# Performance work log

Hardware: AMD Instinct MI355X
Metric: run time of the kernel (lower is better)

Reference implementation:

```python
import jax, jax.numpy as jnp
import numpy as np
import math

D_MODEL = 1024
D_STATE = 64
DT_MIN = 0.001
DT_MAX = 0.1
BATCH = 4
SEQLEN = 4096


def make_hippo_matrix(N):
    P = np.sqrt(1 + 2 * np.arange(N))
    A = P[:, np.newaxis] * P[np.newaxis, :]
    A = np.tril(A) - np.diag(np.arange(N))
    return jnp.asarray(-A, dtype=jnp.float32)


def setup_inputs() -> dict:
    key = jax.random.key(0)
    k_u, k_B, k_C, k_D, k_dt = jax.random.split(key, 5)
    u = jax.random.normal(k_u, (BATCH, SEQLEN, D_MODEL), dtype=jnp.float32)
    A = make_hippo_matrix(D_STATE)  # (N, N) HiPPO-LegS buffer
    B = jax.random.normal(k_B, (D_STATE, 1), dtype=jnp.float32)
    C = jax.random.normal(k_C, (1, D_STATE), dtype=jnp.float32)
    D = jax.random.normal(k_D, (1,), dtype=jnp.float32)
    log_dt = (jax.random.uniform(k_dt, (1,), dtype=jnp.float32)
              * (math.log(DT_MAX) - math.log(DT_MIN)) + math.log(DT_MIN))
    return {"u": u, "A": A, "B": B, "C": C, "D": D, "log_dt": log_dt}


def _forward(u, A, B, C, D, log_dt):
    n = A.shape[0]
    dt = jnp.exp(log_dt)[0]
    A_bar = jax.scipy.linalg.expm(dt * A)                     # (N, N)
    B_bar = jnp.linalg.solve(A, (A_bar - jnp.eye(n, dtype=A.dtype)) @ B)  # (N, 1)
    bvec = B_bar[:, 0]          # (N,)
    cvec = C[0]                 # (N,)
    d_scalar = D[0]
    # Faithful to source: only channel 0 of u drives the SSM.
    u0 = u[:, :, 0]             # (Bn, L)

    def step(x, u_t):
        # x: (Bn, N), u_t: (Bn,)
        x = x @ A_bar.T + u_t[:, None] * bvec
        y = x @ cvec + d_scalar * u_t   # (Bn,)
        return x, y

    x0 = jnp.zeros((u.shape[0], n), dtype=u.dtype)
    _, ys = jax.lax.scan(step, x0, jnp.swapaxes(u0, 0, 1))   # (L, Bn)
    # Scalar output broadcast across all H channels (matches torch expand)
    y = jnp.broadcast_to(jnp.swapaxes(ys, 0, 1)[:, :, None], u.shape)
    return y


def reference(u, A, B, C, D, log_dt):
    return _forward(u, A, B, C, D, log_dt)
```

## Files before the change

### kernel.cpp

```cpp
#include <hip/hip_runtime.h>


#define NT 1024
#define MP 68
#define MB (64 * MP)

typedef __attribute__((ext_vector_type(8))) short v8s;
typedef __attribute__((ext_vector_type(4))) float v4f;

__device__ __forceinline__ unsigned short bf16r(float x) {
  union { float f; unsigned u; } v; v.f = x;
  unsigned r = v.u + 0x7fffu + ((v.u >> 16) & 1u);
  return (unsigned short)(r >> 16);
}
__device__ __forceinline__ float bf2f(unsigned short h) {
  union { unsigned u; float f; } v; v.u = ((unsigned)h) << 16;
  return v.f;
}

__device__ void mm(const float* Ag, const float* Bs, int bT,
                   float* Cd, int cpitch, float* Cd2,
                   int nrt, int nct, int rowbase, int colbase,
                   unsigned short* FRAG) {
  const int t = threadIdx.x;
  __syncthreads();
  {
    const int slot = t >> 1;
    const int jh = (t & 1) * 4;
    const int l = slot & 63;
    const int Tq = slot >> 6;
    const int mrow = (Tq >> 1) * 16 + (l & 15);
    const int kk = (Tq & 1) * 32 + (l >> 4) * 8 + jh;
    const float4 f = *(const float4*)(Ag + mrow * MP + kk);
    ushort4 H, L;
    unsigned short h;
    h = bf16r(f.x); H.x = h; L.x = bf16r(f.x - bf2f(h));
    h = bf16r(f.y); H.y = h; L.y = bf16r(f.y - bf2f(h));
    h = bf16r(f.z); H.z = h; L.z = bf16r(f.z - bf2f(h));
    h = bf16r(f.w); H.w = h; L.w = bf16r(f.w - bf2f(h));
    *(ushort4*)(FRAG + slot * 8 + jh) = H;
    *(ushort4*)(FRAG + 4096 + slot * 8 + jh) = L;
    float y0, y1, y2, y3;
    if (bT) {
      const float4 g = *(const float4*)(Bs + mrow * MP + kk);
      y0 = g.x; y1 = g.y; y2 = g.z; y3 = g.w;
    } else {
      y0 = Bs[(kk + 0) * MP + mrow]; y1 = Bs[(kk + 1) * MP + mrow];
      y2 = Bs[(kk + 2) * MP + mrow]; y3 = Bs[(kk + 3) * MP + mrow];
    }
    h = bf16r(y0); H.x = h; L.x = bf16r(y0 - bf2f(h));
    h = bf16r(y1); H.y = h; L.y = bf16r(y1 - bf2f(h));
    h = bf16r(y2); H.z = h; L.z = bf16r(y2 - bf2f(h));
    h = bf16r(y3); H.w = h; L.w = bf16r(y3 - bf2f(h));
    *(ushort4*)(FRAG + 8192 + slot * 8 + jh) = H;
    *(ushort4*)(FRAG + 12288 + slot * 8 + jh) = L;
  }
  __syncthreads();
  {
    const int w = t >> 6, l = t & 63;
    if (w < 4 && w < nrt) {
      const v8s Ah0 = *(const v8s*)(FRAG + ((w * 2 + 0) * 64 + l) * 8);
      const v8s Ah1 = *(const v8s*)(FRAG + ((w * 2 + 1) * 64 + l) * 8);
      const v8s Al0 = *(const v8s*)(FRAG + 4096 + ((w * 2 + 0) * 64 + l) * 8);
      const v8s Al1 = *(const v8s*)(FRAG + 4096 + ((w * 2 + 1) * 64 + l) * 8);
      for (int Cc = 0; Cc < nct; ++Cc) {
        const v8s Bh0 = *(const v8s*)(FRAG + 8192 + ((Cc * 2 + 0) * 64 + l) * 8);
        const v8s Bh1 = *(const v8s*)(FRAG + 8192 + ((Cc * 2 + 1) * 64 + l) * 8);
        const v8s Bl0 = *(const v8s*)(FRAG + 12288 + ((Cc * 2 + 0) * 64 + l) * 8);
        const v8s Bl1 = *(const v8s*)(FRAG + 12288 + ((Cc * 2 + 1) * 64 + l) * 8);
        v4f acc = {0.f, 0.f, 0.f, 0.f};
        acc = __builtin_amdgcn_mfma_f32_16x16x32_bf16(Ah0, Bh0, acc, 0, 0, 0);
        acc = __builtin_amdgcn_mfma_f32_16x16x32_bf16(Ah1, Bh1, acc, 0, 0, 0);
        acc = __builtin_amdgcn_mfma_f32_16x16x32_bf16(Ah0, Bl0, acc, 0, 0, 0);
        acc = __builtin_amdgcn_mfma_f32_16x16x32_bf16(Ah1, Bl1, acc, 0, 0, 0);
        acc = __builtin_amdgcn_mfma_f32_16x16x32_bf16(Al0, Bh0, acc, 0, 0, 0);
        acc = __builtin_amdgcn_mfma_f32_16x16x32_bf16(Al1, Bh1, acc, 0, 0, 0);
        const int col = colbase + Cc * 16 + (l & 15);
        const int r0 = rowbase + w * 16 + (l >> 4) * 4;
        Cd[(r0 + 0) * cpitch + col] = acc[0];
        Cd[(r0 + 1) * cpitch + col] = acc[1];
        Cd[(r0 + 2) * cpitch + col] = acc[2];
        Cd[(r0 + 3) * cpitch + col] = acc[3];
        if (Cd2) {
          Cd2[(r0 + 0) * MP + col] = acc[0];
          Cd2[(r0 + 1) * MP + col] = acc[1];
          Cd2[(r0 + 2) * MP + col] = acc[2];
          Cd2[(r0 + 3) * MP + col] = acc[3];
        }
      }
    }
  }
  __syncthreads();
}

__device__ __forceinline__ void mv64row(const float* M, const float* vin,
                                        float* vout, float* vscr) {
  __syncthreads();
  const int t = threadIdx.x, i = t & 63, c = t >> 6;
  const float4 m = *(const float4*)(M + i * MP + c * 4);
  vscr[t] = fmaf(m.x, vin[c * 4 + 0], fmaf(m.y, vin[c * 4 + 1],
            fmaf(m.z, vin[c * 4 + 2], m.w * vin[c * 4 + 3])));
  __syncthreads();
  if (t < 64) {
    float s = 0.f;
#pragma unroll
    for (int cc = 0; cc < 16; ++cc) s += vscr[cc * 64 + t];
    vout[t] = s;
  }
  __syncthreads();
}

__device__ __forceinline__ void mv64colT(const float* M, const float* vin,
                                         float* vout, float* vscr) {
  __syncthreads();
  const int t = threadIdx.x, i = t & 63, c = t >> 6;
  float p = 0.f;
#pragma unroll
  for (int j = 0; j < 4; ++j) p = fmaf(M[(c * 4 + j) * MP + i], vin[c * 4 + j], p);
  vscr[t] = p;
  __syncthreads();
  if (t < 64) {
    float s = 0.f;
#pragma unroll
    for (int cc = 0; cc < 16; ++cc) s += vscr[cc * 64 + t];
    vout[t] = s;
  }
  __syncthreads();
}

__device__ void buildG(float* dst, const float* X, const float* X2, const float* X3,
                       float c0, float c1, float c2, float c3, const float* addsrc) {
  __syncthreads();
  for (int e = threadIdx.x; e < MB; e += NT) {
    const int r = e / MP, c = e - r * MP;
    if (c < 64) {
      float v = c1 * X[e] + c2 * X2[e] + c3 * X3[e];
      if (r == c) v += c0;
      if (addsrc) v += addsrc[e];
      dst[e] = v;
    }
  }
  __syncthreads();
}

__global__ __launch_bounds__(NT) void s4_setup(const float* __restrict__ u,
    const float* __restrict__ A, const float* __restrict__ Bv,
    const float* __restrict__ Cv, const float* __restrict__ logdt,
    float* __restrict__ ws) {
  if (blockIdx.x > 0) {
    const int idx = (blockIdx.x - 1) * NT + threadIdx.x;
    ws[4096 + idx] = u[(size_t)idx * 1024];
    return;
  }
  __shared__ __align__(16) float S0[MB];
  __shared__ __align__(16) unsigned short FRAG[16384];
  __shared__ float vB[64], v1[64], v2[64], v3[64], va[64], vb[64], vg[64];
  __shared__ int s_s;
  float* vscr = (float*)FRAG;

  const int t = threadIdx.x;
  float* kbuf = ws;
  float* gX   = ws + 20480;
  float* gX2  = ws + 24832;
  float* gX3  = ws + 29184;
  float* gU0  = ws + 33536;
  float* gU1  = ws + 37888;
  float* gBRT = ws + 42240;
  float* gCQT = ws + 46592;
  const float dt = expf(logdt[0]);

  const float invf[17] = {1.f, 1.f, 1.f / 2.f, 1.f / 6.f, 1.f / 24.f, 1.f / 120.f,
                          1.f / 720.f, 1.f / 5040.f, 1.f / 40320.f, 1.f / 362880.f,
                          1.f / 3628800.f, 1.f / 39916800.f, 1.f / 479001600.f,
                          1.f / 6.2270208e9f, 1.f / 8.71782912e10f,
                          1.f / 1.307674368e12f, 1.f / 2.0922789888e13f};

  {
    const int j = t & 63, ch = t >> 6;
    float p = 0.f;
#pragma unroll
    for (int ii = 0; ii < 4; ++ii) p += fabsf(A[(ch * 4 + ii) * 64 + j]);
    vscr[t] = p;
    __syncthreads();
    if (t < 64) {
      float cs = 0.f;
#pragma unroll
      for (int c = 0; c < 16; ++c) cs += vscr[c * 64 + t];
      cs *= dt;
#pragma unroll
      for (int off = 32; off > 0; off >>= 1) cs = fmaxf(cs, __shfl_xor(cs, off));
      if (t == 0) {
        int s = 0;
        while (cs > 2.0f && s < 30) { cs *= 0.5f; ++s; }
        s_s = s;
      }
    }
    __syncthreads();
  }
  const int sq = s_s;
  const float scl = ldexpf(dt, -sq);

  {
    const float4 a4 = *(const float4*)(A + t * 4);
    float4 x;
    x.x = a4.x * scl; x.y = a4.y * scl; x.z = a4.z * scl; x.w = a4.w * scl;
    const int r = t >> 4, c4 = (t & 15) * 4;
    *(float4*)(S0 + r * MP + c4) = x;
    *(float4*)(gX + r * MP + c4) = x;
  }
  if (t < 64) vB[t] = Bv[t];

  mm(S0, S0, 0, S0, MP, gX2, 4, 4, 0, 0, FRAG);
  mm(gX, S0, 0, gX3, MP, nullptr, 4, 4, 0, 0, FRAG);
  mm(S0, S0, 0, S0, MP, nullptr, 4, 4, 0, 0, FRAG);

  mv64row(gX,  vB, v1, vscr);
  mv64row(gX2, vB, v2, vscr);
  mv64row(gX3, vB, v3, vscr);
  if (t < 64)
    va[t] = invf[13] * vB[t] + invf[14] * v1[t] + invf[15] * v2[t] + invf[16] * v3[t];
  mv64row(S0, va, vb, vscr);
  if (t < 64)
    va[t] = invf[9] * vB[t] + invf[10] * v1[t] + invf[11] * v2[t] + invf[12] * v3[t] + vb[t];
  mv64row(S0, va, vb, vscr);
  if (t < 64)
    va[t] = invf[5] * vB[t] + invf[6] * v1[t] + invf[7] * v2[t] + invf[8] * v3[t] + vb[t];
  mv64row(S0, va, vb, vscr);
  if (t < 64)
    vg[t] = invf[1] * vB[t] + invf[2] * v1[t] + invf[3] * v2[t] + invf[4] * v3[t] + vb[t];

  buildG(gU0, gX, gX2, gX3, invf[12], invf[13], invf[14], invf[15], nullptr);
  mm(gU0, S0, 0, gU1, MP, nullptr, 4, 4, 0, 0, FRAG);
  buildG(gU1, gX, gX2, gX3, invf[8], invf[9], invf[10], invf[11], gU1);
  mm(gU1, S0, 0, gU0, MP, nullptr, 4, 4, 0, 0, FRAG);
  buildG(gU0, gX, gX2, gX3, invf[4], invf[5], invf[6], invf[7], gU0);
  mm(gU0, S0, 0, S0, MP, nullptr, 4, 4, 0, 0, FRAG);
  buildG(S0, gX, gX2, gX3, invf[0], invf[1], invf[2], invf[3], S0);

  for (int it = 0; it < sq; ++it) {
    mv64row(S0, vg, va, vscr);
    if (t < 64) vg[t] = 0.5f * (va[t] + vg[t]);
    mm(S0, S0, 0, S0, MP, nullptr, 4, 4, 0, 0, FRAG);
  }

  __syncthreads();
  if (t < 64) { va[t] = dt * vg[t]; gBRT[t] = dt * vg[t]; }
  {
    float* vc = va; float* vn = vb;
    for (int r = 1; r < 16; ++r) {
      mv64row(S0, vc, vn, vscr);
      if (t < 64) gBRT[r * MP + t] = vn[t];
      float* tmp = vc; vc = vn; vn = tmp;
    }
  }

  mm(S0, S0, 0, S0, MP, nullptr, 4, 4, 0, 0, FRAG);
  mm(S0, S0, 0, S0, MP, nullptr, 4, 4, 0, 0, FRAG);
  mm(S0, S0, 0, S0, MP, nullptr, 4, 4, 0, 0, FRAG);
  mm(S0, S0, 0, S0, MP, nullptr, 4, 4, 0, 0, FRAG);
  mm(gBRT, S0, 1, gBRT, MP, nullptr, 1, 4, 16, 0, FRAG);
  mm(S0, S0, 0, S0, MP, nullptr, 4, 4, 0, 0, FRAG);
  mm(gBRT, S0, 1, gBRT, MP, nullptr, 2, 4, 32, 0, FRAG);
  mm(S0, S0, 0, S0, MP, nullptr, 4, 4, 0, 0, FRAG);

  __syncthreads();
  if (t < 64) { va[t] = Cv[t]; gCQT[t] = Cv[t]; }
  {
    float* vc = va; float* vn = vb;
    for (int qx = 1; qx < 16; ++qx) {
      mv64colT(S0, vc, vn, vscr);
      if (t < 64) gCQT[qx * MP + t] = vn[t];
      float* tmp = vc; vc = vn; vn = tmp;
    }
  }

  mm(S0, S0, 0, S0, MP, nullptr, 4, 4, 0, 0, FRAG);
  mm(S0, S0, 0, S0, MP, nullptr, 4, 4, 0, 0, FRAG);
  mm(S0, S0, 0, S0, MP, nullptr, 4, 4, 0, 0, FRAG);
  mm(S0, S0, 0, S0, MP, nullptr, 4, 4, 0, 0, FRAG);
  mm(gCQT, S0, 0, gCQT, MP, nullptr, 1, 4, 16, 0, FRAG);
  mm(S0, S0, 0, S0, MP, nullptr, 4, 4, 0, 0, FRAG);
  mm(gCQT, S0, 0, gCQT, MP, nullptr, 2, 4, 32, 0, FRAG);

  mm(gCQT, gBRT, 1, kbuf, 64, nullptr, 4, 4, 0, 0, FRAG);
}

__global__ __launch_bounds__(256) void s4_out(const float* __restrict__ ws,
                                              const float* __restrict__ Dp,
                                              float* __restrict__ out) {
  const int bid = blockIdx.x;
  const int b = bid >> 10;
  const int t0 = (bid & 1023) << 2;
  const float* kb = ws;
  const float* ub = ws + 4096 + (b << 12);
  const int tid = threadIdx.x;
  const int t3 = t0 + 3;
  float a0 = 0.f, a1 = 0.f, a2 = 0.f, a3 = 0.f;
  for (int j = tid; j <= t3; j += 256) {
    const float kj = kb[j];
    if (j <= t0)     a0 = fmaf(kj, ub[t0 - j], a0);
    if (j <= t0 + 1) a1 = fmaf(kj, ub[t0 + 1 - j], a1);
    if (j <= t0 + 2) a2 = fmaf(kj, ub[t0 + 2 - j], a2);
    a3 = fmaf(kj, ub[t3 - j], a3);
  }
#pragma unroll
  for (int off = 32; off > 0; off >>= 1) {
    a0 += __shfl_xor(a0, off);
    a1 += __shfl_xor(a1, off);
    a2 += __shfl_xor(a2, off);
    a3 += __shfl_xor(a3, off);
  }
  __shared__ float red[4][4];
  __shared__ float sy[4];
  if ((tid & 63) == 0) {
    const int w = tid >> 6;
    red[0][w] = a0; red[1][w] = a1; red[2][w] = a2; red[3][w] = a3;
  }
  __syncthreads();
  if (tid < 4)
    sy[tid] = red[tid][0] + red[tid][1] + red[tid][2] + red[tid][3] +
              Dp[0] * ub[t0 + tid];
  __syncthreads();
  const int row = tid >> 6, l = tid & 63;
  const float y = sy[row];
  const float4 y4 = make_float4(y, y, y, y);
  float4* dst = (float4*)(out + ((size_t)(b << 12) + t0 + row) * 1024);
  dst[l] = y4; dst[l + 64] = y4; dst[l + 128] = y4; dst[l + 192] = y4;
}

extern "C" void kernel_launch(void* const* d_in, const int* in_sizes, int n_in,
                              void* d_out, int out_size, void* d_ws, size_t ws_size,
                              hipStream_t stream) {
  const float* u  = (const float*)d_in[0];
  const float* A  = (const float*)d_in[1];
  const float* B  = (const float*)d_in[2];
  const float* C  = (const float*)d_in[3];
  const float* D  = (const float*)d_in[4];
  const float* ld = (const float*)d_in[5];
  float* ws = (float*)d_ws;

  s4_setup<<<17, NT, 0, stream>>>(u, A, B, C, ld, ws);
  s4_out<<<4096, 256, 0, stream>>>(ws, D, (float*)d_out);
}
```

Baseline: 169.1 us.

## Shrink setup block to 256 threads and use shuffle-reduced matvecs

Reduces the serial setup kernel block from 1024 to 256 threads (4 waves), so each barrier synchronises fewer waves. Matrix-vector products now reduce partial sums with wave shuffles instead of an LDS scratch pass plus an extra barrier. The MFMA chain is split into three independent accumulators to shorten the dependency chain, and buildG and the fragment conversion are vectorised to cover more work per thread. The grid grows to 65 blocks so the u gather still covers all elements, at the cost of more work per thread in the setup block.

Result: slower. 195.1 us (+15.4%).

```diff
diff --git a/kernel.cpp b/kernel.cpp
--- a/kernel.cpp
+++ b/kernel.cpp
@@ -1,7 +1,7 @@
 #include <hip/hip_runtime.h>
 
 
-#define NT 1024
+#define NT 256
 #define MP 68
 #define MB (64 * MP)
 
@@ -17,6 +17,13 @@
   union { unsigned u; float f; } v; v.u = ((unsigned)h) << 16;
   return v.f;
 }
+__device__ __forceinline__ void cvt4(const float4 f, ushort4* H, ushort4* L) {
+  unsigned short h;
+  h = bf16r(f.x); H->x = h; L->x = bf16r(f.x - bf2f(h));
+  h = bf16r(f.y); H->y = h; L->y = bf16r(f.y - bf2f(h));
+  h = bf16r(f.z); H->z = h; L->z = bf16r(f.z - bf2f(h));
+  h = bf16r(f.w); H->w = h; L->w = bf16r(f.w - bf2f(h));
+}
 
 __device__ void mm(const float* Ag, const float* Bs, int bT,
                    float* Cd, int cpitch, float* Cd2,
@@ -24,41 +31,41 @@
                    unsigned short* FRAG) {
   const int t = threadIdx.x;
   __syncthreads();
-  {
-    const int slot = t >> 1;
-    const int jh = (t & 1) * 4;
-    const int l = slot & 63;
-    const int Tq = slot >> 6;
+  for (int s0 = 0; s0 < 512; s0 += 256) {
+    const int s = s0 + t;
+    const int l = s & 63, Tq = s >> 6;
     const int mrow = (Tq >> 1) * 16 + (l & 15);
-    const int kk = (Tq & 1) * 32 + (l >> 4) * 8 + jh;
-    const float4 f = *(const float4*)(Ag + mrow * MP + kk);
-    ushort4 H, L;
-    unsigned short h;
-    h = bf16r(f.x); H.x = h; L.x = bf16r(f.x - bf2f(h));
-    h = bf16r(f.y); H.y = h; L.y = bf16r(f.y - bf2f(h));
-    h = bf16r(f.z); H.z = h; L.z = bf16r(f.z - bf2f(h));
-    h = bf16r(f.w); H.w = h; L.w = bf16r(f.w - bf2f(h));
-    *(ushort4*)(FRAG + slot * 8 + jh) = H;
-    *(ushort4*)(FRAG + 4096 + slot * 8 + jh) = L;
-    float y0, y1, y2, y3;
+    const int kk = (Tq & 1) * 32 + (l >> 4) * 8;
+    const float* ap = Ag + mrow * MP + kk;
+    const float4 f0 = *(const float4*)ap;
+    const float4 f1 = *(const float4*)(ap + 4);
+    ushort4 H0, L0, H1, L1;
+    cvt4(f0, &H0, &L0); cvt4(f1, &H1, &L1);
+    *(ushort4*)(FRAG + s * 8)            = H0;
+    *(ushort4*)(FRAG + s * 8 + 4)        = H1;
+    *(ushort4*)(FRAG + 4096 + s * 8)     = L0;
+    *(ushort4*)(FRAG + 4096 + s * 8 + 4) = L1;
+    float4 g0, g1;
     if (bT) {
-      const float4 g = *(const float4*)(Bs + mrow * MP + kk);
-      y0 = g.x; y1 = g.y; y2 = g.z; y3 = g.w;
+      const float* bp = Bs + mrow * MP + kk;
+      g0 = *(const float4*)bp;
+      g1 = *(const float4*)(bp + 4);
     } else {
-      y0 = Bs[(kk + 0) * MP + mrow]; y1 = Bs[(kk + 1) * MP + mrow];
-      y2 = Bs[(kk + 2) * MP + mrow]; y3 = Bs[(kk + 3) * MP + mrow];
-    }
-    h = bf16r(y0); H.x = h; L.x = bf16r(y0 - bf2f(h));
-    h = bf16r(y1); H.y = h; L.y = bf16r(y1 - bf2f(h));
-    h = bf16r(y2); H.z = h; L.z = bf16r(y2 - bf2f(h));
-    h = bf16r(y3); H.w = h; L.w = bf16r(y3 - bf2f(h));
-    *(ushort4*)(FRAG + 8192 + slot * 8 + jh) = H;
-    *(ushort4*)(FRAG + 12288 + slot * 8 + jh) = L;
+      g0.x = Bs[(kk + 0) * MP + mrow]; g0.y = Bs[(kk + 1) * MP + mrow];
+      g0.z = Bs[(kk + 2) * MP + mrow]; g0.w = Bs[(kk + 3) * MP + mrow];
+      g1.x = Bs[(kk + 4) * MP + mrow]; g1.y = Bs[(kk + 5) * MP + mrow];
+      g1.z = Bs[(kk + 6) * MP + mrow]; g1.w = Bs[(kk + 7) * MP + mrow];
+    }
+    cvt4(g0, &H0, &L0); cvt4(g1, &H1, &L1);
+    *(ushort4*)(FRAG + 8192 + s * 8)      = H0;
+    *(ushort4*)(FRAG + 8192 + s * 8 + 4)  = H1;
+    *(ushort4*)(FRAG + 12288 + s * 8)     = L0;
+    *(ushort4*)(FRAG + 12288 + s * 8 + 4) = L1;
   }
   __syncthreads();
   {
     const int w = t >> 6, l = t & 63;
-    if (w < 4 && w < nrt) {
+    if (w < nrt) {
       const v8s Ah0 = *(const v8s*)(FRAG + ((w * 2 + 0) * 64 + l) * 8);
       const v8s Ah1 = *(const v8s*)(FRAG + ((w * 2 + 1) * 64 + l) * 8);
       const v8s Al0 = *(const v8s*)(FRAG + 4096 + ((w * 2 + 0) * 64 + l) * 8);
@@ -68,24 +75,28 @@
         const v8s Bh1 = *(const v8s*)(FRAG + 8192 + ((Cc * 2 + 1) * 64 + l) * 8);
         const v8s Bl0 = *(const v8s*)(FRAG + 12288 + ((Cc * 2 + 0) * 64 + l) * 8);
         const v8s Bl1 = *(const v8s*)(FRAG + 12288 + ((Cc * 2 + 1) * 64 + l) * 8);
-        v4f acc = {0.f, 0.f, 0.f, 0.f};
-        acc = __builtin_amdgcn_mfma_f32_16x16x32_bf16(Ah0, Bh0, acc, 0, 0, 0);
-        acc = __builtin_amdgcn_mfma_f32_16x16x32_bf16(Ah1, Bh1, acc, 0, 0, 0);
-        acc = __builtin_amdgcn_mfma_f32_16x16x32_bf16(Ah0, Bl0, acc, 0, 0, 0);
-        acc = __builtin_amdgcn_mfma_f32_16x16x32_bf16(Ah1, Bl1, acc, 0, 0, 0);
-        acc = __builtin_amdgcn_mfma_f32_16x16x32_bf16(Al0, Bh0, acc, 0, 0, 0);
-        acc = __builtin_amdgcn_mfma_f32_16x16x32_bf16(Al1, Bh1, acc, 0, 0, 0);
+        const v4f z = {0.f, 0.f, 0.f, 0.f};
+        v4f a0 = __builtin_amdgcn_mfma_f32_16x16x32_bf16(Ah0, Bh0, z, 0, 0, 0);
+        a0 = __builtin_amdgcn_mfma_f32_16x16x32_bf16(Ah1, Bh1, a0, 0, 0, 0);
+        v4f a1 = __builtin_amdgcn_mfma_f32_16x16x32_bf16(Ah0, Bl0, z, 0, 0, 0);
+        a1 = __builtin_amdgcn_mfma_f32_16x16x32_bf16(Ah1, Bl1, a1, 0, 0, 0);
+        v4f a2 = __builtin_amdgcn_mfma_f32_16x16x32_bf16(Al0, Bh0, z, 0, 0, 0);
+        a2 = __builtin_amdgcn_mfma_f32_16x16x32_bf16(Al1, Bh1, a2, 0, 0, 0);
         const int col = colbase + Cc * 16 + (l & 15);
         const int r0 = rowbase + w * 16 + (l >> 4) * 4;
-        Cd[(r0 + 0) * cpitch + col] = acc[0];
-        Cd[(r0 + 1) * cpitch + col] = acc[1];
-        Cd[(r0 + 2) * cpitch + col] = acc[2];
-        Cd[(r0 + 3) * cpitch + col] = acc[3];
+        const float o0 = a0[0] + a1[0] + a2[0];
+        const float o1 = a0[1] + a1[1] + a2[1];
+        const float o2 = a0[2] + a1[2] + a2[2];
+        const float o3 = a0[3] + a1[3] + a2[3];
+        Cd[(r0 + 0) * cpitch + col] = o0;
+        Cd[(r0 + 1) * cpitch + col] = o1;
+        Cd[(r0 + 2) * cpitch + col] = o2;
+        Cd[(r0 + 3) * cpitch + col] = o3;
         if (Cd2) {
-          Cd2[(r0 + 0) * MP + col] = acc[0];
-          Cd2[(r0 + 1) * MP + col] = acc[1];
-          Cd2[(r0 + 2) * MP + col] = acc[2];
-          Cd2[(r0 + 3) * MP + col] = acc[3];
+          Cd2[(r0 + 0) * MP + col] = o0;
+          Cd2[(r0 + 1) * MP + col] = o1;
+          Cd2[(r0 + 2) * MP + col] = o2;
+          Cd2[(r0 + 3) * MP + col] = o3;
         }
       }
     }
@@ -94,51 +105,77 @@
 }
 
 __device__ __forceinline__ void mv64row(const float* M, const float* vin,
-                                        float* vout, float* vscr) {
-  __syncthreads();
-  const int t = threadIdx.x, i = t & 63, c = t >> 6;
-  const float4 m = *(const float4*)(M + i * MP + c * 4);
-  vscr[t] = fmaf(m.x, vin[c * 4 + 0], fmaf(m.y, vin[c * 4 + 1],
-            fmaf(m.z, vin[c * 4 + 2], m.w * vin[c * 4 + 3])));
-  __syncthreads();
-  if (t < 64) {
-    float s = 0.f;
-#pragma unroll
-    for (int cc = 0; cc < 16; ++cc) s += vscr[cc * 64 + t];
-    vout[t] = s;
+                                        float* vout, float* out2, int half) {
+  const int t = threadIdx.x;
+  __syncthreads();
+  const int w = t >> 6, l = t & 63;
+  const int row = w * 16 + (l >> 2), q = l & 3;
+  const float* mp = M + row * MP + q * 16;
+  const float* vp = vin + q * 16;
+  float p = 0.f;
+#pragma unroll
+  for (int j = 0; j < 16; j += 4) {
+    const float4 m = *(const float4*)(mp + j);
+    p = fmaf(m.x, vp[j + 0], p);
+    p = fmaf(m.y, vp[j + 1], p);
+    p = fmaf(m.z, vp[j + 2], p);
+    p = fmaf(m.w, vp[j + 3], p);
+  }
+  p += __shfl_xor(p, 1);
+  p += __shfl_xor(p, 2);
+  if (q == 0) {
+    float s = half ? 0.5f * (p + vin[row]) : p;
+    vout[row] = s;
+    if (out2) out2[row] = s;
   }
   __syncthreads();
 }
 
 __device__ __forceinline__ void mv64colT(const float* M, const float* vin,
-                                         float* vout, float* vscr) {
-  __syncthreads();
-  const int t = threadIdx.x, i = t & 63, c = t >> 6;
+                                         float* vout, float* out2) {
+  const int t = threadIdx.x;
+  __syncthreads();
+  const int w = t >> 6, l = t & 63;
+  const int col = w * 16 + (l >> 2), q = l & 3;
   float p = 0.f;
 #pragma unroll
-  for (int j = 0; j < 4; ++j) p = fmaf(M[(c * 4 + j) * MP + i], vin[c * 4 + j], p);
-  vscr[t] = p;
-  __syncthreads();
-  if (t < 64) {
-    float s = 0.f;
-#pragma unroll
-    for (int cc = 0; cc < 16; ++cc) s += vscr[cc * 64 + t];
-    vout[t] = s;
+  for (int j = 0; j < 16; ++j)
+    p = fmaf(M[(q * 16 + j) * MP + col], vin[q * 16 + j], p);
+  p += __shfl_xor(p, 1);
+  p += __shfl_xor(p, 2);
+  if (q == 0) {
+    vout[col] = p;
+    if (out2) out2[col] = p;
   }
   __syncthreads();
 }
 
 __device__ void buildG(float* dst, const float* X, const float* X2, const float* X3,
                        float c0, float c1, float c2, float c3, const float* addsrc) {
-  __syncthreads();
-  for (int e = threadIdx.x; e < MB; e += NT) {
-    const int r = e / MP, c = e - r * MP;
-    if (c < 64) {
-      float v = c1 * X[e] + c2 * X2[e] + c3 * X3[e];
-      if (r == c) v += c0;
-      if (addsrc) v += addsrc[e];
-      dst[e] = v;
-    }
+  const int t = threadIdx.x;
+  __syncthreads();
+  const int r = t >> 2, cb = (t & 3) * 16;
+#pragma unroll
+  for (int j = 0; j < 16; j += 4) {
+    const int c = cb + j;
+    const int e = r * MP + c;
+    const float4 x1 = *(const float4*)(X + e);
+    const float4 x2 = *(const float4*)(X2 + e);
+    const float4 x3 = *(const float4*)(X3 + e);
+    float4 v;
+    v.x = fmaf(c1, x1.x, fmaf(c2, x2.x, c3 * x3.x));
+    v.y = fmaf(c1, x1.y, fmaf(c2, x2.y, c3 * x3.y));
+    v.z = fmaf(c1, x1.z, fmaf(c2, x2.z, c3 * x3.z));
+    v.w = fmaf(c1, x1.w, fmaf(c2, x2.w, c3 * x3.w));
+    if (r == c + 0) v.x += c0;
+    if (r == c + 1) v.y += c0;
+    if (r == c + 2) v.z += c0;
+    if (r == c + 3) v.w += c0;
+    if (addsrc) {
+      const float4 a = *(const float4*)(addsrc + e);
+      v.x += a.x; v.y += a.y; v.z += a.z; v.w += a.w;
+    }
+    *(float4*)(dst + e) = v;
   }
   __syncthreads();
 }
@@ -176,16 +213,14 @@
                           1.f / 1.307674368e12f, 1.f / 2.0922789888e13f};
 
   {
-    const int j = t & 63, ch = t >> 6;
+    const int j = t & 63, w = t >> 6;
     float p = 0.f;
 #pragma unroll
-    for (int ii = 0; ii < 4; ++ii) p += fabsf(A[(ch * 4 + ii) * 64 + j]);
+    for (int ii = 0; ii < 16; ++ii) p += fabsf(A[(w * 16 + ii) * 64 + j]);
     vscr[t] = p;
     __syncthreads();
     if (t < 64) {
-      float cs = 0.f;
-#pragma unroll
-      for (int c = 0; c < 16; ++c) cs += vscr[c * 64 + t];
+      float cs = vscr[t] + vscr[64 + t] + vscr[128 + t] + vscr[192 + t];
       cs *= dt;
 #pragma unroll
       for (int off = 32; off > 0; off >>= 1) cs = fmaxf(cs, __shfl_xor(cs, off));
@@ -201,33 +236,41 @@
   const float scl = ldexpf(dt, -sq);
 
   {
-    const float4 a4 = *(const float4*)(A + t * 4);
-    float4 x;
-    x.x = a4.x * scl; x.y = a4.y * scl; x.z = a4.z * scl; x.w = a4.w * scl;
-    const int r = t >> 4, c4 = (t & 15) * 4;
-    *(float4*)(S0 + r * MP + c4) = x;
-    *(float4*)(gX + r * MP + c4) = x;
-  }
-  if (t < 64) vB[t] = Bv[t];
+    const int r = t >> 2, cb = (t & 3) * 16;
+#pragma unroll
+    for (int j = 0; j < 16; j += 4) {
+      const float4 a4 = *(const float4*)(A + r * 64 + cb + j);
+      float4 x;
+      x.x = a4.x * scl; x.y = a4.y * scl; x.z = a4.z * scl; x.w = a4.w * scl;
+      *(float4*)(S0 + r * MP + cb + j) = x;
+      *(float4*)(gX + r * MP + cb + j) = x;
+    }
+    if (t < 64) vB[t] = Bv[t];
+    __syncthreads();
+  }
 
   mm(S0, S0, 0, S0, MP, gX2, 4, 4, 0, 0, FRAG);
   mm(gX, S0, 0, gX3, MP, nullptr, 4, 4, 0, 0, FRAG);
   mm(S0, S0, 0, S0, MP, nullptr, 4, 4, 0, 0, FRAG);
 
-  mv64row(gX,  vB, v1, vscr);
-  mv64row(gX2, vB, v2, vscr);
-  mv64row(gX3, vB, v3, vscr);
+  mv64row(gX,  vB, v1, nullptr, 0);
+  mv64row(gX2, vB, v2, nullptr, 0);
+  mv64row(gX3, vB, v3, nullptr, 0);
   if (t < 64)
     va[t] = invf[13] * vB[t] + invf[14] * v1[t] + invf[15] * v2[t] + invf[16] * v3[t];
-  mv64row(S0, va, vb, vscr);
+  __syncthreads();
+  mv64row(S0, va, vb, nullptr, 0);
   if (t < 64)
     va[t] = invf[9] * vB[t] + invf[10] * v1[t] + invf[11] * v2[t] + invf[12] * v3[t] + vb[t];
-  mv64row(S0, va, vb, vscr);
+  __syncthreads();
+  mv64row(S0, va, vb, nullptr, 0);
   if (t < 64)
     va[t] = invf[5] * vB[t] + invf[6] * v1[t] + invf[7] * v2[t] + invf[8] * v3[t] + vb[t];
-  mv64row(S0, va, vb, vscr);
+  __syncthreads();
+  mv64row(S0, va, vb, nullptr, 0);
   if (t < 64)
     vg[t] = invf[1] * vB[t] + invf[2] * v1[t] + invf[3] * v2[t] + invf[4] * v3[t] + vb[t];
+  __syncthreads();
 
   buildG(gU0, gX, gX2, gX3, invf[12], invf[13], invf[14], invf[15], nullptr);
   mm(gU0, S0, 0, gU1, MP, nullptr, 4, 4, 0, 0, FRAG);
@@ -237,19 +280,24 @@
   mm(gU0, S0, 0, S0, MP, nullptr, 4, 4, 0, 0, FRAG);
   buildG(S0, gX, gX2, gX3, invf[0], invf[1], invf[2], invf[3], S0);
 
+  float* vcur = vg;
+  float* vnxt = va;
   for (int it = 0; it < sq; ++it) {
-    mv64row(S0, vg, va, vscr);
-    if (t < 64) vg[t] = 0.5f * (va[t] + vg[t]);
+    mv64row(S0, vcur, vnxt, nullptr, 1);
+    { float* tmp = vcur; vcur = vnxt; vnxt = tmp; }
     mm(S0, S0, 0, S0, MP, nullptr, 4, 4, 0, 0, FRAG);
   }
 
-  __syncthreads();
-  if (t < 64) { va[t] = dt * vg[t]; gBRT[t] = dt * vg[t]; }
-  {
-    float* vc = va; float* vn = vb;
+  if (t < 64) {
+    const float bb = dt * vcur[t];
+    v1[t] = bb;
+    gBRT[t] = bb;
+  }
+  __syncthreads();
+  {
+    float* vc = v1; float* vn = v2;
     for (int r = 1; r < 16; ++r) {
-      mv64row(S0, vc, vn, vscr);
-      if (t < 64) gBRT[r * MP + t] = vn[t];
+      mv64row(S0, vc, vn, gBRT + r * MP, 0);
       float* tmp = vc; vc = vn; vn = tmp;
     }
   }
@@ -263,13 +311,16 @@
   mm(gBRT, S0, 1, gBRT, MP, nullptr, 2, 4, 32, 0, FRAG);
   mm(S0, S0, 0, S0, MP, nullptr, 4, 4, 0, 0, FRAG);
 
-  __syncthreads();
-  if (t < 64) { va[t] = Cv[t]; gCQT[t] = Cv[t]; }
-  {
-    float* vc = va; float* vn = vb;
+  if (t < 64) {
+    const float cc = Cv[t];
+    v1[t] = cc;
+    gCQT[t] = cc;
+  }
+  __syncthreads();
+  {
+    float* vc = v1; float* vn = v2;
     for (int qx = 1; qx < 16; ++qx) {
-      mv64colT(S0, vc, vn, vscr);
-      if (t < 64) gCQT[qx * MP + t] = vn[t];
+      mv64colT(S0, vc, vn, gCQT + qx * MP);
       float* tmp = vc; vc = vn; vn = tmp;
     }
   }
@@ -339,6 +390,6 @@
   const float* ld = (const float*)d_in[5];
   float* ws = (float*)d_ws;
 
-  s4_setup<<<17, NT, 0, stream>>>(u, A, B, C, ld, ws);
+  s4_setup<<<65, NT, 0, stream>>>(u, A, B, C, ld, ws);
   s4_out<<<4096, 256, 0, stream>>>(ws, D, (float*)d_out);
 }
```
